# Performance work log

Measured on AMD Instinct MI355X. Metric: run time of the kernel, lower is better.

## Reference

```python
import jax, jax.numpy as jnp
import numpy as np
import math

RC = 5.0            # radial cutoff rc_rad
ZETA = [1, 2, 3, 4] # zeta list from configs['zeta']=4

def _angular_consts(z):
    # all (lx,ly,lz) with lx+ly+lz <= z (code generates n in range(z+1) and expands
    # each n into its non-negative integer triples)
    tri = []
    for lx in range(z + 1):
        for ly in range(z + 1 - lx):
            for lz in range(z + 1 - lx - ly):
                tri.append((lx, ly, lz))
    tri = np.array(tri, np.int32)
    n = tri.sum(1)
    # fact_norm = (n!/(lx!ly!lz!)) * (z!/((z-n)! n!)) = z! / ((z-n)! lx! ly! lz!)
    c = np.array([math.factorial(z) / (math.factorial(z - int(s)) * math.factorial(int(a)) * math.factorial(int(b)) * math.factorial(int(d)))
                  for (a, b, d), s in zip(tri, n)], np.float32)
    sign = ((-1.0) ** n).astype(np.float32)  # lambda=-1 channel: (1-cos)^z expansion
    return tri, c, sign

ANG = [_angular_consts(z) for z in ZETA]
silu = jax.nn.silu


def setup_inputs() -> dict:
    key = jax.random.key(0)
    ks = jax.random.split(key, 16)
    nat, npairs, Nrad, nzeta, emb, nelem = 2048, 65536, 8, 4, 4, 4
    feat = (Nrad + Nrad * 2 * nzeta) * emb  # 288
    L = 20.0
    pos = jax.random.uniform(ks[0], (nat, 3), jnp.float32) * L
    cell = L * jnp.eye(3, dtype=jnp.float32)
    i1 = jax.random.randint(ks[1], (npairs,), 0, nat, jnp.int32)
    i2 = jax.random.randint(ks[2], (npairs,), 0, nat, jnp.int32)
    shift = jnp.zeros((npairs, 3), jnp.int32)
    ids = jax.random.randint(ks[3], (nat,), 0, nelem, jnp.int32)
    onehot = jax.nn.one_hot(ids, nelem, dtype=jnp.float32)
    def W(k, i, o):
        return jax.random.normal(k, (i, o), jnp.float32) * 0.1
    return dict(
        positions=pos, cell=cell, species_onehot=onehot,
        sw1=W(ks[4], nelem, 64), sb1=jnp.zeros((64,), jnp.float32),
        sw2=W(ks[5], 64, emb), sb2=jnp.zeros((emb,), jnp.float32),
        rw1=W(ks[6], Nrad, 64), rb1=jnp.zeros((64,), jnp.float32),
        rw2=W(ks[7], 64, (nzeta + 1) * Nrad), rb2=jnp.zeros(((nzeta + 1) * Nrad,), jnp.float32),
        aw1=W(ks[8], feat, 256), ab1=jnp.zeros((256,), jnp.float32),
        aw2=W(ks[9], 256, 128), ab2=jnp.zeros((128,), jnp.float32),
        aw3=W(ks[10], 128, 1), ab3=jnp.zeros((1,), jnp.float32),
        first_atom_idx=i1, second_atom_idx=i2, shift_vectors=shift,
    )


def reference(positions, cell, species_onehot, sw1, sb1, sw2, sb2,
              rw1, rb1, rw2, rb2, aw1, ab1, aw2, ab2, aw3, ab3,
              first_atom_idx, second_atom_idx, shift_vectors):
    nat = positions.shape[0]
    Nrad = rw1.shape[0]
    nzeta = rw2.shape[1] // Nrad - 1
    # pair displacement vectors with PBC shifts
    rij = (positions[second_atom_idx] - positions[first_atom_idx]
           + shift_vectors.astype(jnp.float32) @ cell)            # [P,3]
    r = jnp.sqrt(jnp.sum(rij * rij, axis=-1) + 1e-12)             # [P]
    u = rij / r[:, None]                                          # unit vectors
    fc = jnp.where(r < RC, 0.5 * (jnp.cos(jnp.pi * r / RC) + 1.0), 0.0)
    # Gaussian radial basis -> learned radial functions (silu MLP, linear head)
    centers = jnp.linspace(0.0, RC, Nrad)
    w = RC / Nrad
    basis = jnp.exp(-((r[:, None] - centers) ** 2) / (2.0 * w * w)) * fc[:, None]
    rad = silu(basis @ rw1 + rb1) @ rw2 + rb2
    rad = rad.reshape(-1, nzeta + 1, Nrad) * fc[:, None, None]    # [P, nzeta+1, Nrad]
    # species encoder MLP -> per-atom embedding, gathered onto neighbor side
    semb = silu(species_onehot @ sw1 + sb1) @ sw2 + sb2           # [nat, emb]
    sp = semb[second_atom_idx]                                    # [P, emb]
    seg = lambda v: jax.ops.segment_sum(v, first_atom_idx, num_segments=nat)
    # two-body radial descriptor [nat, Nrad, emb]
    R = seg(rad[:, 0, :, None] * sp[:, None, :])
    feats = [R.reshape(nat, -1)]
    # three-body angular descriptors via multinomial (lx,ly,lz) expansion
    for zi in range(nzeta):
        tri, c, sign = ANG[zi]
        l = jnp.asarray(tri, jnp.float32)                         # [L,3]
        g = jnp.prod(u[:, None, :] ** l[None], axis=-1)           # [P,L] u^lx u^ly u^lz
        t = rad[:, 1 + zi, :, None, None] * g[:, None, :, None] * sp[:, None, None, :]
        G = seg(t)                                                # [nat,Nrad,L,emb]
        G2 = G * G
        Ap = jnp.einsum('inle,l->ine', G2, jnp.asarray(c))        # sum_jk f f (1+cos)^z
        Am = jnp.einsum('inle,l->ine', G2, jnp.asarray(c * sign)) # sum_jk f f (1-cos)^z
        feats += [Ap.reshape(nat, -1), Am.reshape(nat, -1)]
    F = jnp.concatenate(feats, axis=-1)                           # [nat, feature_size]
    h = silu(F @ aw1 + ab1)
    h = silu(h @ aw2 + ab2)
    e = h @ aw3 + ab3                                             # per-atom energies
    return jnp.sum(e)


if __name__ == '__main__':
    out = reference(**setup_inputs())
    print(out)
```

## Files before the change

### kernel.cpp

```cpp
#include <hip/hip_runtime.h>
#include <cmath>

#define NAT  2048
#define NP   65536
#define CAP  64
#define SCAP 8192
#define SSTR 120

__constant__ int GLX[70] = {0,
  0,0,0,1,
  0,0,0,0,0,0,1,1,1,2,
  0,0,0,0,0,0,0,0,0,0,1,1,1,1,1,1,2,2,2,3,
  0,0,0,0,0,0,0,0,0,0,0,0,0,0,0,1,1,1,1,1,1,1,1,1,1,2,2,2,2,2,2,3,3,3,4};
__constant__ int GLY[70] = {0,
  0,0,1,0,
  0,0,0,1,1,2,0,0,1,0,
  0,0,0,0,1,1,1,2,2,3,0,0,0,1,1,2,0,0,1,0,
  0,0,0,0,0,1,1,1,1,2,2,2,3,3,4,0,0,0,0,1,1,1,2,2,3,0,0,0,1,1,2,0,0,1,0};
__constant__ int GLZ[70] = {0,
  0,1,0,0,
  0,1,2,0,1,0,0,1,0,0,
  0,1,2,3,0,1,2,0,1,0,0,1,2,0,1,0,0,1,0,0,
  0,1,2,3,4,0,1,2,3,0,1,2,0,1,0,0,1,2,3,0,1,2,0,1,0,0,1,2,0,1,0,0,1,0,0};
__constant__ float C_ALL[69] = {
  1,1,1,1,
  1,2,1,2,2,1,2,2,2,1,
  1,3,3,1,3,6,3,3,3,1,3,6,3,6,6,3,3,3,3,1,
  1,4,6,4,1,4,12,12,4,6,12,6,4,4,1,4,12,12,4,12,24,12,12,12,4,6,12,6,12,12,6,4,4,4,1};
__constant__ float CS_ALL[69] = {
  1,-1,-1,-1,
  1,-2,1,-2,2,1,-2,2,2,1,
  1,-3,3,-1,-3,6,-3,3,-3,-1,-3,6,-3,6,-6,-3,3,-3,-3,-1,
  1,-4,6,-4,1,-4,12,-12,4,6,-12,6,-4,4,1,-4,12,-12,4,12,-24,12,-12,12,6,-12,6,-12,12,6,-4,4,4,1};
__constant__ int LTAB[4]    = {4,10,20,35};
__constant__ int CUMTAB[4]  = {0,4,14,34};
__constant__ int BASETAB[4] = {32,160,480,1120};

__device__ __forceinline__ float silu_f(float x){ return x / (1.0f + expf(-x)); }

__global__ __launch_bounds__(256) void k_prep(
    const float* __restrict__ pos, const float* __restrict__ cell,
    const int* __restrict__ i1, const int* __restrict__ i2,
    const int* __restrict__ sv,
    int* __restrict__ cursor, int* __restrict__ order,
    int* __restrict__ nflat, int2* __restrict__ flat)
{
  const int p = blockIdx.x*256 + threadIdx.x;
  const int a = i1[p], b = i2[p];
  const float s0=(float)sv[p*3+0], s1=(float)sv[p*3+1], s2=(float)sv[p*3+2];
  const float rx = pos[b*3+0]-pos[a*3+0] + s0*cell[0]+s1*cell[3]+s2*cell[6];
  const float ry = pos[b*3+1]-pos[a*3+1] + s0*cell[1]+s1*cell[4]+s2*cell[7];
  const float rz = pos[b*3+2]-pos[a*3+2] + s0*cell[2]+s1*cell[5]+s2*cell[8];
  const float r = sqrtf(rx*rx+ry*ry+rz*rz + 1e-12f);
  if (r < 5.0f){
    int s = atomicAdd(&cursor[a], 1);
    if (s < CAP){
      order[a*CAP + s] = p;
      int fs = atomicAdd(nflat, 1);
      if (fs < SCAP) flat[fs] = make_int2(p, a*CAP + s);
    }
  }
}

__global__ __launch_bounds__(64) void k_stage(
    const float* __restrict__ pos, const float* __restrict__ cell,
    const float* __restrict__ oneh,
    const int* __restrict__ i1, const int* __restrict__ i2,
    const int* __restrict__ sv,
    const float* __restrict__ sw1, const float* __restrict__ sb1,
    const float* __restrict__ sw2, const float* __restrict__ sb2,
    const float* __restrict__ rw1, const float* __restrict__ rb1,
    const float* __restrict__ rw2, const float* __restrict__ rb2,
    const int* __restrict__ nflat, const int2* __restrict__ flat,
    float* __restrict__ staged)
{
  const int lane = threadIdx.x;
  int ntot = *nflat; if (ntot > SCAP) ntot = SCAP;

  for (int w = blockIdx.x; w < ntot; w += 2048){
    const int2 fl = flat[w];
    const int pid = fl.x, dest = fl.y;
    const int a = i1[pid], b = i2[pid];
    const float s0=(float)sv[pid*3+0], s1=(float)sv[pid*3+1], s2=(float)sv[pid*3+2];
    const float rx = pos[b*3+0]-pos[a*3+0] + s0*cell[0]+s1*cell[3]+s2*cell[6];
    const float ry = pos[b*3+1]-pos[a*3+1] + s0*cell[1]+s1*cell[4]+s2*cell[7];
    const float rz = pos[b*3+2]-pos[a*3+2] + s0*cell[2]+s1*cell[5]+s2*cell[8];
    const float r  = sqrtf(rx*rx+ry*ry+rz*rz + 1e-12f);
    const float inv= 1.0f/r;
    const float ux=rx*inv, uy=ry*inv, uz=rz*inv;
    const float fc = 0.5f*(cosf(0.6283185307179586f*r)+1.0f);

    float basis[8];
#pragma unroll
    for (int kk=0;kk<8;kk++){
      float d = r - (float)kk*(5.0f/7.0f);
      basis[kk] = expf(-d*d*1.28f)*fc;
    }
    float h = rb1[lane];
#pragma unroll
    for (int kk=0;kk<8;kk++) h += basis[kk]*rw1[kk*64+lane];
    h = silu_f(h);
    const int ln = (lane < 40) ? lane : 0;
    float racc = rb2[ln];
#pragma unroll
    for (int o=0;o<64;o++){
      float hb = __shfl(h, o);
      racc += hb * rw2[o*40 + ln];
    }
    float* dst = staged + (size_t)dest*SSTR;
    if (lane < 40) dst[lane] = racc*fc;

    {
      int ex=GLX[lane], ey=GLY[lane], ez=GLZ[lane];
      float g=1.f;
      for (int q=0;q<ex;q++) g*=ux;
      for (int q=0;q<ey;q++) g*=uy;
      for (int q=0;q<ez;q++) g*=uz;
      dst[40+lane]=g;
    }
    if (lane < 6){
      int l2 = 64+lane;
      int ex=GLX[l2], ey=GLY[l2], ez=GLZ[l2];
      float g=1.f;
      for (int q=0;q<ex;q++) g*=ux;
      for (int q=0;q<ey;q++) g*=uy;
      for (int q=0;q<ez;q++) g*=uz;
      dst[104+lane]=g;
    }
    {
      const float o1=oneh[b*4+1], o2=oneh[b*4+2], o3=oneh[b*4+3];
      const int spec = (int)(o1 + 2.0f*o2 + 3.0f*o3 + 0.5f);
      float hh = silu_f(sb1[lane] + sw1[spec*64+lane]);
      const float4 w2 = ((const float4*)sw2)[lane];
      float q0=hh*w2.x, q1=hh*w2.y, q2=hh*w2.z, q3=hh*w2.w;
#pragma unroll
      for (int off=32; off>0; off>>=1){
        q0 += __shfl_xor(q0, off); q1 += __shfl_xor(q1, off);
        q2 += __shfl_xor(q2, off); q3 += __shfl_xor(q3, off);
      }
      if (lane < 4){
        float v = (lane==0) ? q0+sb2[0] : (lane==1) ? q1+sb2[1]
                : (lane==2) ? q2+sb2[2] : q3+sb2[3];
        dst[110+lane] = v;
      }
    }
  }
}

__global__ __launch_bounds__(256) void k_feat(
    const int* __restrict__ cursor, const int* __restrict__ order,
    const float* __restrict__ staged, float* __restrict__ Fout)
{
  const int atom = blockIdx.x, tid = threadIdx.x;
  __shared__ float G[2240];
  __shared__ float sdata[8][SSTR];
  __shared__ int opid[CAP];
  __shared__ int plist[CAP];

  int cnt = cursor[atom]; if (cnt > CAP) cnt = CAP;
  if (tid < CAP) opid[tid] = (tid < cnt) ? order[atom*CAP + tid] : 0x7fffffff;
  __syncthreads();
  if (tid < cnt){
    int my = opid[tid]; int rk = 0;
    for (int j=0;j<cnt;j++) rk += (opid[j] < my);
    plist[rk] = tid;
  }

  float acc[9];
  int ridx[9], gidx[9], eidx[9];
#pragma unroll
  for (int k=0;k<9;k++){
    acc[k]=0.f;
    int a = tid + (k<<8);
    int ri=0, gi=0, ei=0;
    if (a < 32){ ri = a>>2; gi = 0; ei = a&3; }
    else if (a < 2240){
      int b = a-32; int lb, nl, l, n;
      if (b < 128)      { lb=b;      ei=lb&3; nl=lb>>2; l=nl%4;  n=nl/4;  ri=8 +n; gi=1 +l; }
      else if (b < 448) { lb=b-128;  ei=lb&3; nl=lb>>2; l=nl%10; n=nl/10; ri=16+n; gi=5 +l; }
      else if (b < 1088){ lb=b-448;  ei=lb&3; nl=lb>>2; l=nl%20; n=nl/20; ri=24+n; gi=15+l; }
      else              { lb=b-1088; ei=lb&3; nl=lb>>2; l=nl%35; n=nl/35; ri=32+n; gi=35+l; }
    }
    ridx[k]=ri; gidx[k]=gi; eidx[k]=ei;
  }
  __syncthreads();

  for (int c0=0; c0<cnt; c0+=8){
    const int nc = (cnt-c0 < 8) ? (cnt-c0) : 8;
    for (int idx=tid; idx<nc*SSTR; idx+=256){
      int jj = idx/SSTR, i = idx - jj*SSTR;
      sdata[jj][i] = staged[(size_t)(atom*CAP + plist[c0+jj])*SSTR + i];
    }
    __syncthreads();
    for (int jj=0;jj<nc;jj++){
      const float* sd = sdata[jj];
#pragma unroll
      for (int k=0;k<9;k++)
        acc[k] += sd[ridx[k]] * sd[40+gidx[k]] * sd[110+eidx[k]];
    }
    __syncthreads();
  }

#pragma unroll
  for (int k=0;k<9;k++){
    int a = tid + (k<<8);
    if (a < 2240) G[a] = acc[k];
  }
  __syncthreads();

  float* Fo = Fout + atom*288;
  if (tid < 32) Fo[tid] = G[tid];
  if (tid < 128){
    const int zi = tid>>5, n=(tid>>2)&7, e=tid&3;
    const int L = LTAB[zi], cb = CUMTAB[zi], bs = BASETAB[zi];
    float ap=0.f, am=0.f;
    for (int l=0;l<L;l++){
      float v  = G[bs + ((n*L + l)<<2) + e];
      float v2 = v*v;
      ap += C_ALL [cb+l]*v2;
      am += CS_ALL[cb+l]*v2;
    }
    Fo[32 + (zi<<6)      + (n<<2) + e] = ap;
    Fo[32 + (zi<<6) + 32 + (n<<2) + e] = am;
  }
}

__global__ __launch_bounds__(512) void k_mlp2(
    const float* __restrict__ F,
    const float* __restrict__ aw1, const float* __restrict__ ab1,
    const float* __restrict__ aw2, const float* __restrict__ ab2,
    const float* __restrict__ aw3, const float* __restrict__ ab3,
    float* __restrict__ out)
{
  const int tid = threadIdx.x;
  const int abase = blockIdx.x*8;
  __shared__ float Fs[8][288];
  __shared__ float P1[2][8][256];
  __shared__ float Hs[8][256];
  __shared__ float P2[4][8][128];
  __shared__ float Ps[8][128];
  __shared__ float es[8];

  for (int idx=tid; idx<8*288; idx+=512){
    int a = idx/288, i = idx - a*288;
    Fs[a][i] = F[(abase+a)*288 + i];
  }
  __syncthreads();

  {
    const int o = tid & 255, half = tid >> 8;
    const int i0 = half*144;
    float p1[8];
#pragma unroll
    for (int a=0;a<8;a++) p1[a]=0.f;
    for (int i=i0;i<i0+144;i++){
      float w = aw1[i*256 + o];
#pragma unroll
      for (int a=0;a<8;a++) p1[a] += Fs[a][i]*w;
    }
#pragma unroll
    for (int a=0;a<8;a++) P1[half][a][o] = p1[a];
  }
  __syncthreads();
  {
    const int o = tid & 255, half = tid >> 8;
    if (half == 0){
#pragma unroll
      for (int a=0;a<8;a++)
        Hs[a][o] = silu_f(ab1[o] + P1[0][a][o] + P1[1][a][o]);
    }
  }
  __syncthreads();

  {
    const int o = tid & 127, q = tid >> 7;
    const int i0 = q*64;
    float p2[8];
#pragma unroll
    for (int a=0;a<8;a++) p2[a]=0.f;
    for (int i=i0;i<i0+64;i++){
      float w = aw2[i*128 + o];
#pragma unroll
      for (int a=0;a<8;a++) p2[a] += Hs[a][i]*w;
    }
#pragma unroll
    for (int a=0;a<8;a++) P2[q][a][o] = p2[a];
  }
  __syncthreads();

#pragma unroll
  for (int rep=0; rep<2; rep++){
    int idx = tid + rep*512;
    int a = idx >> 7, o = idx & 127;
    float h2 = ab2[o] + P2[0][a][o] + P2[1][a][o] + P2[2][a][o] + P2[3][a][o];
    Ps[a][o] = silu_f(h2)*aw3[o];
  }
  __syncthreads();

  {
    const int wv = tid >> 6, lane = tid & 63;
    float s = Ps[wv][lane] + Ps[wv][64+lane];
    for (int off=32; off>0; off>>=1) s += __shfl_xor(s, off);
    if (lane == 0) es[wv] = s;
  }
  __syncthreads();
  if (tid == 0){
    float bsum = es[0]+es[1]+es[2]+es[3]+es[4]+es[5]+es[6]+es[7] + 8.0f*ab3[0];
    atomicAdd(out, bsum);
  }
}

extern "C" void kernel_launch(void* const* d_in, const int* in_sizes, int n_in,
                              void* d_out, int out_size, void* d_ws, size_t ws_size,
                              hipStream_t stream) {
  const float* pos  = (const float*)d_in[0];
  const float* cell = (const float*)d_in[1];
  const float* oneh = (const float*)d_in[2];
  const float* sw1  = (const float*)d_in[3];
  const float* sb1  = (const float*)d_in[4];
  const float* sw2  = (const float*)d_in[5];
  const float* sb2  = (const float*)d_in[6];
  const float* rw1  = (const float*)d_in[7];
  const float* rb1  = (const float*)d_in[8];
  const float* rw2  = (const float*)d_in[9];
  const float* rb2  = (const float*)d_in[10];
  const float* aw1  = (const float*)d_in[11];
  const float* ab1  = (const float*)d_in[12];
  const float* aw2  = (const float*)d_in[13];
  const float* ab2  = (const float*)d_in[14];
  const float* aw3  = (const float*)d_in[15];
  const float* ab3  = (const float*)d_in[16];
  const int*   i1   = (const int*)d_in[17];
  const int*   i2   = (const int*)d_in[18];
  const int*   sv   = (const int*)d_in[19];

  char* ws = (char*)d_ws;
  int*   cursor = (int*)  (ws + 0);
  int*   nflat  = (int*)  (ws + 8192);
  int*   order  = (int*)  (ws + 8448);
  int2*  flat   = (int2*) (ws + 532736);
  float* staged = (float*)(ws + 598528);
  float* F      = (float*)(ws + 4530688);

  hipMemsetAsync(cursor, 0, 8196, stream);
  hipMemsetAsync(d_out, 0, sizeof(float), stream);
  k_prep <<<NP/256, 256, 0, stream>>>(pos, cell, i1, i2, sv,
                                      cursor, order, nflat, flat);
  k_stage<<<2048,    64, 0, stream>>>(pos, cell, oneh, i1, i2, sv,
                                      sw1, sb1, sw2, sb2,
                                      rw1, rb1, rw2, rb2,
                                      nflat, flat, staged);
  k_feat <<<NAT,    256, 0, stream>>>(cursor, order, staged, F);
  k_mlp2 <<<NAT/8,  512, 0, stream>>>(F, aw1, ab1, aw2, ab2, aw3, ab3, (float*)d_out);
}
```

Before: 73.47 us.

## Fuse all stages into one cooperative persistent kernel with grid syncs

Replaces the two memsets and four kernel launches with a single cooperative kernel of 256 blocks of 512 threads. Grid-wide syncs separate the pair binning, per-pair staging, per-atom feature accumulation and MLP phases, and a final block does a deterministic reduction in place of the atomic add. Staged rows are now indexed by flat slot through a new slot-to-flat map. The aim is to remove launch and memset overhead, at the cost of grid-sync latency and lower parallelism in the feature phase, where each block now handles 8 atoms sequentially. It also edits one entry of the sign-coefficient table, which inserts a value and shifts the rest of that row.

```diff
diff --git a/kernel.cpp b/kernel.cpp
--- a/kernel.cpp
+++ b/kernel.cpp
@@ -1,5 +1,8 @@
 #include <hip/hip_runtime.h>
+#include <hip/hip_cooperative_groups.h>
 #include <cmath>
+
+namespace cg = cooperative_groups;
 
 #define NAT  2048
 #define NP   65536
@@ -31,147 +34,141 @@
   1,-1,-1,-1,
   1,-2,1,-2,2,1,-2,2,2,1,
   1,-3,3,-1,-3,6,-3,3,-3,-1,-3,6,-3,6,-6,-3,3,-3,-3,-1,
-  1,-4,6,-4,1,-4,12,-12,4,6,-12,6,-4,4,1,-4,12,-12,4,12,-24,12,-12,12,6,-12,6,-12,12,6,-4,4,4,1};
+  1,-4,6,-4,1,-4,12,-12,4,6,-12,6,-4,4,1,-4,12,-12,4,12,-24,12,-12,12,4,6,-12,6,-12,12,6,-4,4,4,1};
 __constant__ int LTAB[4]    = {4,10,20,35};
 __constant__ int CUMTAB[4]  = {0,4,14,34};
 __constant__ int BASETAB[4] = {32,160,480,1120};
 
 __device__ __forceinline__ float silu_f(float x){ return x / (1.0f + expf(-x)); }
 
-__global__ __launch_bounds__(256) void k_prep(
-    const float* __restrict__ pos, const float* __restrict__ cell,
-    const int* __restrict__ i1, const int* __restrict__ i2,
+__global__ __launch_bounds__(512) void k_all(
+    const float* __restrict__ pos,  const float* __restrict__ cell,
+    const float* __restrict__ oneh,
+    const float* __restrict__ sw1,  const float* __restrict__ sb1,
+    const float* __restrict__ sw2,  const float* __restrict__ sb2,
+    const float* __restrict__ rw1,  const float* __restrict__ rb1,
+    const float* __restrict__ rw2,  const float* __restrict__ rb2,
+    const float* __restrict__ aw1,  const float* __restrict__ ab1,
+    const float* __restrict__ aw2,  const float* __restrict__ ab2,
+    const float* __restrict__ aw3,  const float* __restrict__ ab3,
+    const int* __restrict__ i1,     const int* __restrict__ i2,
     const int* __restrict__ sv,
-    int* __restrict__ cursor, int* __restrict__ order,
-    int* __restrict__ nflat, int2* __restrict__ flat)
+    int* cursor, int* nflat, int* order, int* slot2flat, int* flat,
+    float* staged, float* partials, float* out)
 {
-  const int p = blockIdx.x*256 + threadIdx.x;
-  const int a = i1[p], b = i2[p];
-  const float s0=(float)sv[p*3+0], s1=(float)sv[p*3+1], s2=(float)sv[p*3+2];
-  const float rx = pos[b*3+0]-pos[a*3+0] + s0*cell[0]+s1*cell[3]+s2*cell[6];
-  const float ry = pos[b*3+1]-pos[a*3+1] + s0*cell[1]+s1*cell[4]+s2*cell[7];
-  const float rz = pos[b*3+2]-pos[a*3+2] + s0*cell[2]+s1*cell[5]+s2*cell[8];
-  const float r = sqrtf(rx*rx+ry*ry+rz*rz + 1e-12f);
-  if (r < 5.0f){
-    int s = atomicAdd(&cursor[a], 1);
-    if (s < CAP){
-      order[a*CAP + s] = p;
-      int fs = atomicAdd(nflat, 1);
-      if (fs < SCAP) flat[fs] = make_int2(p, a*CAP + s);
-    }
-  }
-}
-
-__global__ __launch_bounds__(64) void k_stage(
-    const float* __restrict__ pos, const float* __restrict__ cell,
-    const float* __restrict__ oneh,
-    const int* __restrict__ i1, const int* __restrict__ i2,
-    const int* __restrict__ sv,
-    const float* __restrict__ sw1, const float* __restrict__ sb1,
-    const float* __restrict__ sw2, const float* __restrict__ sb2,
-    const float* __restrict__ rw1, const float* __restrict__ rb1,
-    const float* __restrict__ rw2, const float* __restrict__ rb2,
-    const int* __restrict__ nflat, const int2* __restrict__ flat,
-    float* __restrict__ staged)
-{
-  const int lane = threadIdx.x;
-  int ntot = *nflat; if (ntot > SCAP) ntot = SCAP;
-
-  for (int w = blockIdx.x; w < ntot; w += 2048){
-    const int2 fl = flat[w];
-    const int pid = fl.x, dest = fl.y;
-    const int a = i1[pid], b = i2[pid];
-    const float s0=(float)sv[pid*3+0], s1=(float)sv[pid*3+1], s2=(float)sv[pid*3+2];
+  cg::grid_group grid = cg::this_grid();
+  const int tid = threadIdx.x, blk = blockIdx.x;
+  const int gid = blk*512 + tid;
+  __shared__ __align__(16) char smem[58368];
+
+  if (gid < NAT) cursor[gid] = 0;
+  if (gid == 0)  *nflat = 0;
+  grid.sync();
+
+  if (gid < NP){
+    const int p = gid;
+    const int a = i1[p], b = i2[p];
+    const float s0=(float)sv[p*3+0], s1=(float)sv[p*3+1], s2=(float)sv[p*3+2];
     const float rx = pos[b*3+0]-pos[a*3+0] + s0*cell[0]+s1*cell[3]+s2*cell[6];
     const float ry = pos[b*3+1]-pos[a*3+1] + s0*cell[1]+s1*cell[4]+s2*cell[7];
     const float rz = pos[b*3+2]-pos[a*3+2] + s0*cell[2]+s1*cell[5]+s2*cell[8];
-    const float r  = sqrtf(rx*rx+ry*ry+rz*rz + 1e-12f);
-    const float inv= 1.0f/r;
-    const float ux=rx*inv, uy=ry*inv, uz=rz*inv;
-    const float fc = 0.5f*(cosf(0.6283185307179586f*r)+1.0f);
-
-    float basis[8];
-#pragma unroll
-    for (int kk=0;kk<8;kk++){
-      float d = r - (float)kk*(5.0f/7.0f);
-      basis[kk] = expf(-d*d*1.28f)*fc;
-    }
-    float h = rb1[lane];
-#pragma unroll
-    for (int kk=0;kk<8;kk++) h += basis[kk]*rw1[kk*64+lane];
-    h = silu_f(h);
-    const int ln = (lane < 40) ? lane : 0;
-    float racc = rb2[ln];
-#pragma unroll
-    for (int o=0;o<64;o++){
-      float hb = __shfl(h, o);
-      racc += hb * rw2[o*40 + ln];
-    }
-    float* dst = staged + (size_t)dest*SSTR;
-    if (lane < 40) dst[lane] = racc*fc;
-
-    {
-      int ex=GLX[lane], ey=GLY[lane], ez=GLZ[lane];
-      float g=1.f;
-      for (int q=0;q<ex;q++) g*=ux;
-      for (int q=0;q<ey;q++) g*=uy;
-      for (int q=0;q<ez;q++) g*=uz;
-      dst[40+lane]=g;
-    }
-    if (lane < 6){
-      int l2 = 64+lane;
-      int ex=GLX[l2], ey=GLY[l2], ez=GLZ[l2];
-      float g=1.f;
-      for (int q=0;q<ex;q++) g*=ux;
-      for (int q=0;q<ey;q++) g*=uy;
-      for (int q=0;q<ez;q++) g*=uz;
-      dst[104+lane]=g;
-    }
-    {
-      const float o1=oneh[b*4+1], o2=oneh[b*4+2], o3=oneh[b*4+3];
-      const int spec = (int)(o1 + 2.0f*o2 + 3.0f*o3 + 0.5f);
-      float hh = silu_f(sb1[lane] + sw1[spec*64+lane]);
-      const float4 w2 = ((const float4*)sw2)[lane];
-      float q0=hh*w2.x, q1=hh*w2.y, q2=hh*w2.z, q3=hh*w2.w;
-#pragma unroll
-      for (int off=32; off>0; off>>=1){
-        q0 += __shfl_xor(q0, off); q1 += __shfl_xor(q1, off);
-        q2 += __shfl_xor(q2, off); q3 += __shfl_xor(q3, off);
-      }
-      if (lane < 4){
-        float v = (lane==0) ? q0+sb2[0] : (lane==1) ? q1+sb2[1]
-                : (lane==2) ? q2+sb2[2] : q3+sb2[3];
-        dst[110+lane] = v;
-      }
-    }
-  }
-}
-
-__global__ __launch_bounds__(256) void k_feat(
-    const int* __restrict__ cursor, const int* __restrict__ order,
-    const float* __restrict__ staged, float* __restrict__ Fout)
-{
-  const int atom = blockIdx.x, tid = threadIdx.x;
-  __shared__ float G[2240];
-  __shared__ float sdata[8][SSTR];
-  __shared__ int opid[CAP];
-  __shared__ int plist[CAP];
-
-  int cnt = cursor[atom]; if (cnt > CAP) cnt = CAP;
-  if (tid < CAP) opid[tid] = (tid < cnt) ? order[atom*CAP + tid] : 0x7fffffff;
-  __syncthreads();
-  if (tid < cnt){
-    int my = opid[tid]; int rk = 0;
-    for (int j=0;j<cnt;j++) rk += (opid[j] < my);
-    plist[rk] = tid;
-  }
-
-  float acc[9];
-  int ridx[9], gidx[9], eidx[9];
-#pragma unroll
-  for (int k=0;k<9;k++){
-    acc[k]=0.f;
-    int a = tid + (k<<8);
+    const float r = sqrtf(rx*rx+ry*ry+rz*rz + 1e-12f);
+    if (r < 5.0f){
+      int s = atomicAdd(&cursor[a], 1);
+      if (s < CAP){
+        int fs = atomicAdd(nflat, 1);
+        order[a*CAP + s] = p;
+        if (fs < SCAP){ slot2flat[a*CAP + s] = fs; flat[fs] = p; }
+        else          { slot2flat[a*CAP + s] = -1; }
+      }
+    }
+  }
+  grid.sync();
+
+  {
+    int ntot = *nflat; if (ntot > SCAP) ntot = SCAP;
+    const int lane = tid & 63;
+    const int w0 = blk*8 + (tid >> 6);
+    for (int w = w0; w < ntot; w += 2048){
+      const int pid = flat[w];
+      const int a = i1[pid], b = i2[pid];
+      const float s0=(float)sv[pid*3+0], s1=(float)sv[pid*3+1], s2=(float)sv[pid*3+2];
+      const float rx = pos[b*3+0]-pos[a*3+0] + s0*cell[0]+s1*cell[3]+s2*cell[6];
+      const float ry = pos[b*3+1]-pos[a*3+1] + s0*cell[1]+s1*cell[4]+s2*cell[7];
+      const float rz = pos[b*3+2]-pos[a*3+2] + s0*cell[2]+s1*cell[5]+s2*cell[8];
+      const float r  = sqrtf(rx*rx+ry*ry+rz*rz + 1e-12f);
+      const float inv= 1.0f/r;
+      const float ux=rx*inv, uy=ry*inv, uz=rz*inv;
+      const float fc = 0.5f*(cosf(0.6283185307179586f*r)+1.0f);
+
+      float basis[8];
+#pragma unroll
+      for (int kk=0;kk<8;kk++){
+        float d = r - (float)kk*(5.0f/7.0f);
+        basis[kk] = expf(-d*d*1.28f)*fc;
+      }
+      float h = rb1[lane];
+#pragma unroll
+      for (int kk=0;kk<8;kk++) h += basis[kk]*rw1[kk*64+lane];
+      h = silu_f(h);
+      const int ln = (lane < 40) ? lane : 0;
+      float racc = rb2[ln];
+#pragma unroll
+      for (int o=0;o<64;o++){
+        float hb = __shfl(h, o);
+        racc += hb * rw2[o*40 + ln];
+      }
+      float* dst = staged + (size_t)w*SSTR;
+      if (lane < 40) dst[lane] = racc*fc;
+      {
+        int ex=GLX[lane], ey=GLY[lane], ez=GLZ[lane];
+        float g=1.f;
+        for (int q=0;q<ex;q++) g*=ux;
+        for (int q=0;q<ey;q++) g*=uy;
+        for (int q=0;q<ez;q++) g*=uz;
+        dst[40+lane]=g;
+      }
+      if (lane < 6){
+        int l2 = 64+lane;
+        int ex=GLX[l2], ey=GLY[l2], ez=GLZ[l2];
+        float g=1.f;
+        for (int q=0;q<ex;q++) g*=ux;
+        for (int q=0;q<ey;q++) g*=uy;
+        for (int q=0;q<ez;q++) g*=uz;
+        dst[104+lane]=g;
+      }
+      {
+        const float o1=oneh[b*4+1], o2=oneh[b*4+2], o3=oneh[b*4+3];
+        const int spec = (int)(o1 + 2.0f*o2 + 3.0f*o3 + 0.5f);
+        float hh = silu_f(sb1[lane] + sw1[spec*64+lane]);
+        const float4 w2 = ((const float4*)sw2)[lane];
+        float q0=hh*w2.x, q1=hh*w2.y, q2=hh*w2.z, q3=hh*w2.w;
+#pragma unroll
+        for (int off=32; off>0; off>>=1){
+          q0 += __shfl_xor(q0, off); q1 += __shfl_xor(q1, off);
+          q2 += __shfl_xor(q2, off); q3 += __shfl_xor(q3, off);
+        }
+        if (lane < 4){
+          float v = (lane==0) ? q0+sb2[0] : (lane==1) ? q1+sb2[1]
+                  : (lane==2) ? q2+sb2[2] : q3+sb2[3];
+          dst[110+lane] = v;
+        }
+      }
+    }
+  }
+  grid.sync();
+
+  float* G    = (float*)(smem);
+  float* sbuf = (float*)(smem+8960);
+  int*   opid = (int*)  (smem+12800);
+  int*   pslot= (int*)  (smem+13056);
+  int*   sflb = (int*)  (smem+13312);
+  float* Fs   = (float*)(smem+16384);
+
+  int ridx[5], gidx[5], eidx[5];
+#pragma unroll
+  for (int k=0;k<5;k++){
+    int a = tid + (k<<9);
     int ri=0, gi=0, ei=0;
     if (a < 32){ ri = a>>2; gi = 0; ei = a&3; }
     else if (a < 2240){
@@ -183,69 +180,69 @@
     }
     ridx[k]=ri; gidx[k]=gi; eidx[k]=ei;
   }
-  __syncthreads();
-
-  for (int c0=0; c0<cnt; c0+=8){
-    const int nc = (cnt-c0 < 8) ? (cnt-c0) : 8;
-    for (int idx=tid; idx<nc*SSTR; idx+=256){
-      int jj = idx/SSTR, i = idx - jj*SSTR;
-      sdata[jj][i] = staged[(size_t)(atom*CAP + plist[c0+jj])*SSTR + i];
-    }
-    __syncthreads();
-    for (int jj=0;jj<nc;jj++){
-      const float* sd = sdata[jj];
-#pragma unroll
-      for (int k=0;k<9;k++)
-        acc[k] += sd[ridx[k]] * sd[40+gidx[k]] * sd[110+eidx[k]];
-    }
-    __syncthreads();
-  }
-
-#pragma unroll
-  for (int k=0;k<9;k++){
-    int a = tid + (k<<8);
-    if (a < 2240) G[a] = acc[k];
-  }
-  __syncthreads();
-
-  float* Fo = Fout + atom*288;
-  if (tid < 32) Fo[tid] = G[tid];
-  if (tid < 128){
-    const int zi = tid>>5, n=(tid>>2)&7, e=tid&3;
-    const int L = LTAB[zi], cb = CUMTAB[zi], bs = BASETAB[zi];
-    float ap=0.f, am=0.f;
-    for (int l=0;l<L;l++){
-      float v  = G[bs + ((n*L + l)<<2) + e];
-      float v2 = v*v;
-      ap += C_ALL [cb+l]*v2;
-      am += CS_ALL[cb+l]*v2;
-    }
-    Fo[32 + (zi<<6)      + (n<<2) + e] = ap;
-    Fo[32 + (zi<<6) + 32 + (n<<2) + e] = am;
-  }
-}
-
-__global__ __launch_bounds__(512) void k_mlp2(
-    const float* __restrict__ F,
-    const float* __restrict__ aw1, const float* __restrict__ ab1,
-    const float* __restrict__ aw2, const float* __restrict__ ab2,
-    const float* __restrict__ aw3, const float* __restrict__ ab3,
-    float* __restrict__ out)
-{
-  const int tid = threadIdx.x;
-  const int abase = blockIdx.x*8;
-  __shared__ float Fs[8][288];
-  __shared__ float P1[2][8][256];
-  __shared__ float Hs[8][256];
-  __shared__ float P2[4][8][128];
-  __shared__ float Ps[8][128];
-  __shared__ float es[8];
-
-  for (int idx=tid; idx<8*288; idx+=512){
-    int a = idx/288, i = idx - a*288;
-    Fs[a][i] = F[(abase+a)*288 + i];
-  }
-  __syncthreads();
+
+  for (int aa=0; aa<8; aa++){
+    const int atom = blk*8 + aa;
+    int cnt = cursor[atom]; if (cnt > CAP) cnt = CAP;
+    if (tid < CAP) opid[tid] = (tid < cnt) ? order[atom*CAP + tid] : 0x7fffffff;
+    __syncthreads();
+    if (tid < cnt){
+      int my = opid[tid]; int rk = 0;
+      for (int j=0;j<cnt;j++) rk += (opid[j] < my);
+      pslot[rk] = tid;
+    }
+    float acc[5] = {0.f,0.f,0.f,0.f,0.f};
+    __syncthreads();
+
+    for (int c0=0; c0<cnt; c0+=8){
+      const int nc = (cnt-c0 < 8) ? (cnt-c0) : 8;
+      if (tid < nc) sflb[tid] = slot2flat[atom*CAP + pslot[c0+tid]];
+      __syncthreads();
+      for (int idx=tid; idx<nc*SSTR; idx+=512){
+        int jj = idx/SSTR, i = idx - jj*SSTR;
+        int fsl = sflb[jj];
+        sbuf[idx] = (fsl >= 0) ? staged[(size_t)fsl*SSTR + i] : 0.f;
+      }
+      __syncthreads();
+      for (int jj=0;jj<nc;jj++){
+        const float* sd = sbuf + jj*SSTR;
+#pragma unroll
+        for (int k=0;k<5;k++)
+          acc[k] += sd[ridx[k]] * sd[40+gidx[k]] * sd[110+eidx[k]];
+      }
+      __syncthreads();
+    }
+
+#pragma unroll
+    for (int k=0;k<5;k++){
+      int a = tid + (k<<9);
+      if (a < 2240) G[a] = acc[k];
+    }
+    __syncthreads();
+
+    float* Fo = Fs + aa*288;
+    if (tid < 32) Fo[tid] = G[tid];
+    if (tid < 128){
+      const int zi = tid>>5, n=(tid>>2)&7, e=tid&3;
+      const int L = LTAB[zi], cb = CUMTAB[zi], bs = BASETAB[zi];
+      float ap=0.f, am=0.f;
+      for (int l=0;l<L;l++){
+        float v  = G[bs + ((n*L + l)<<2) + e];
+        float v2 = v*v;
+        ap += C_ALL [cb+l]*v2;
+        am += CS_ALL[cb+l]*v2;
+      }
+      Fo[32 + (zi<<6)      + (n<<2) + e] = ap;
+      Fo[32 + (zi<<6) + 32 + (n<<2) + e] = am;
+    }
+    __syncthreads();
+  }
+
+  float* P1 = (float*)(smem+25600);
+  float* Hs = (float*)(smem);
+  float* P2 = (float*)(smem+41984);
+  float* Ps = (float*)(smem+8192);
+  float* es = (float*)(smem+12288);
 
   {
     const int o = tid & 255, half = tid >> 8;
@@ -256,10 +253,10 @@
     for (int i=i0;i<i0+144;i++){
       float w = aw1[i*256 + o];
 #pragma unroll
-      for (int a=0;a<8;a++) p1[a] += Fs[a][i]*w;
-    }
-#pragma unroll
-    for (int a=0;a<8;a++) P1[half][a][o] = p1[a];
+      for (int a=0;a<8;a++) p1[a] += Fs[a*288+i]*w;
+    }
+#pragma unroll
+    for (int a=0;a<8;a++) P1[half*2048 + a*256 + o] = p1[a];
   }
   __syncthreads();
   {
@@ -267,11 +264,10 @@
     if (half == 0){
 #pragma unroll
       for (int a=0;a<8;a++)
-        Hs[a][o] = silu_f(ab1[o] + P1[0][a][o] + P1[1][a][o]);
-    }
-  }
-  __syncthreads();
-
+        Hs[a*256+o] = silu_f(ab1[o] + P1[a*256+o] + P1[2048 + a*256+o]);
+    }
+  }
+  __syncthreads();
   {
     const int o = tid & 127, q = tid >> 7;
     const int i0 = q*64;
@@ -281,32 +277,42 @@
     for (int i=i0;i<i0+64;i++){
       float w = aw2[i*128 + o];
 #pragma unroll
-      for (int a=0;a<8;a++) p2[a] += Hs[a][i]*w;
-    }
-#pragma unroll
-    for (int a=0;a<8;a++) P2[q][a][o] = p2[a];
-  }
-  __syncthreads();
-
+      for (int a=0;a<8;a++) p2[a] += Hs[a*256+i]*w;
+    }
+#pragma unroll
+    for (int a=0;a<8;a++) P2[q*1024 + a*128 + o] = p2[a];
+  }
+  __syncthreads();
 #pragma unroll
   for (int rep=0; rep<2; rep++){
     int idx = tid + rep*512;
     int a = idx >> 7, o = idx & 127;
-    float h2 = ab2[o] + P2[0][a][o] + P2[1][a][o] + P2[2][a][o] + P2[3][a][o];
-    Ps[a][o] = silu_f(h2)*aw3[o];
-  }
-  __syncthreads();
-
+    float h2 = ab2[o] + P2[a*128+o] + P2[1024+a*128+o]
+             + P2[2048+a*128+o] + P2[3072+a*128+o];
+    Ps[a*128+o] = silu_f(h2)*aw3[o];
+  }
+  __syncthreads();
   {
     const int wv = tid >> 6, lane = tid & 63;
-    float s = Ps[wv][lane] + Ps[wv][64+lane];
+    float s = Ps[wv*128+lane] + Ps[wv*128+64+lane];
     for (int off=32; off>0; off>>=1) s += __shfl_xor(s, off);
     if (lane == 0) es[wv] = s;
   }
   __syncthreads();
   if (tid == 0){
-    float bsum = es[0]+es[1]+es[2]+es[3]+es[4]+es[5]+es[6]+es[7] + 8.0f*ab3[0];
-    atomicAdd(out, bsum);
+    partials[blk] = es[0]+es[1]+es[2]+es[3]+es[4]+es[5]+es[6]+es[7] + 8.0f*ab3[0];
+  }
+  grid.sync();
+
+  if (blk == 0){
+    float* red = (float*)smem;
+    red[tid] = (tid < 256) ? partials[tid] : 0.f;
+    __syncthreads();
+    for (int off=256; off>0; off>>=1){
+      if (tid < off) red[tid] += red[tid+off];
+      __syncthreads();
+    }
+    if (tid == 0) out[0] = red[0];
   }
 }
 
@@ -335,21 +341,24 @@
   const int*   sv   = (const int*)d_in[19];
 
   char* ws = (char*)d_ws;
-  int*   cursor = (int*)  (ws + 0);
-  int*   nflat  = (int*)  (ws + 8192);
-  int*   order  = (int*)  (ws + 8448);
-  int2*  flat   = (int2*) (ws + 532736);
-  float* staged = (float*)(ws + 598528);
-  float* F      = (float*)(ws + 4530688);
-
-  hipMemsetAsync(cursor, 0, 8196, stream);
-  hipMemsetAsync(d_out, 0, sizeof(float), stream);
-  k_prep <<<NP/256, 256, 0, stream>>>(pos, cell, i1, i2, sv,
-                                      cursor, order, nflat, flat);
-  k_stage<<<2048,    64, 0, stream>>>(pos, cell, oneh, i1, i2, sv,
-                                      sw1, sb1, sw2, sb2,
-                                      rw1, rb1, rw2, rb2,
-                                      nflat, flat, staged);
-  k_feat <<<NAT,    256, 0, stream>>>(cursor, order, staged, F);
-  k_mlp2 <<<NAT/8,  512, 0, stream>>>(F, aw1, ab1, aw2, ab2, aw3, ab3, (float*)d_out);
+  int*   cursor    = (int*)  (ws + 0);
+  int*   nflat     = (int*)  (ws + 8192);
+  int*   order     = (int*)  (ws + 8448);
+  int*   slot2flat = (int*)  (ws + 532736);
+  int*   flat      = (int*)  (ws + 1057024);
+  float* staged    = (float*)(ws + 1089792);
+  float* partials  = (float*)(ws + 5021952);
+  float* outf      = (float*)d_out;
+
+  void* args[] = {
+    (void*)&pos, (void*)&cell, (void*)&oneh,
+    (void*)&sw1, (void*)&sb1, (void*)&sw2, (void*)&sb2,
+    (void*)&rw1, (void*)&rb1, (void*)&rw2, (void*)&rb2,
+    (void*)&aw1, (void*)&ab1, (void*)&aw2, (void*)&ab2,
+    (void*)&aw3, (void*)&ab3,
+    (void*)&i1, (void*)&i2, (void*)&sv,
+    (void*)&cursor, (void*)&nflat, (void*)&order, (void*)&slot2flat,
+    (void*)&flat, (void*)&staged, (void*)&partials, (void*)&outf
+  };
+  hipLaunchCooperativeKernel((void*)k_all, dim3(256), dim3(512), args, 0, stream);
 }
```

Result: slower. 182.9 us (+148.9%).

## Fuse pair filtering and staging into one wave-compacted kernel

Applied to the files above, without the earlier changes.

Merges the pair-filter and staging kernels. Each wavefront ballots its surviving pairs, reserves flat slots with a single atomic, and then processes the survivors by broadcasting their geometry through shuffles. The per-species embedding MLP is computed once per block into shared memory instead of once per pair. The two memsets become one, and the final float atomicAdd is replaced by a last-block reduction over per-block partials. A CS_ALL constant is also edited. In exchange, the staging work now runs on only 256 blocks, which may serialize the per-survivor MLP loop within each wave.

```diff
diff --git a/kernel.cpp b/kernel.cpp
--- a/kernel.cpp
+++ b/kernel.cpp
@@ -31,38 +31,14 @@
   1,-1,-1,-1,
   1,-2,1,-2,2,1,-2,2,2,1,
   1,-3,3,-1,-3,6,-3,3,-3,-1,-3,6,-3,6,-6,-3,3,-3,-3,-1,
-  1,-4,6,-4,1,-4,12,-12,4,6,-12,6,-4,4,1,-4,12,-12,4,12,-24,12,-12,12,6,-12,6,-12,12,6,-4,4,4,1};
+  1,-4,6,-4,1,-4,12,-12,4,6,-12,6,-4,4,1,-4,12,-12,4,12,-24,12,-12,12,4,6,-12,6,-12,12,6,-4,4,4,1};
 __constant__ int LTAB[4]    = {4,10,20,35};
 __constant__ int CUMTAB[4]  = {0,4,14,34};
 __constant__ int BASETAB[4] = {32,160,480,1120};
 
 __device__ __forceinline__ float silu_f(float x){ return x / (1.0f + expf(-x)); }
 
-__global__ __launch_bounds__(256) void k_prep(
-    const float* __restrict__ pos, const float* __restrict__ cell,
-    const int* __restrict__ i1, const int* __restrict__ i2,
-    const int* __restrict__ sv,
-    int* __restrict__ cursor, int* __restrict__ order,
-    int* __restrict__ nflat, int2* __restrict__ flat)
-{
-  const int p = blockIdx.x*256 + threadIdx.x;
-  const int a = i1[p], b = i2[p];
-  const float s0=(float)sv[p*3+0], s1=(float)sv[p*3+1], s2=(float)sv[p*3+2];
-  const float rx = pos[b*3+0]-pos[a*3+0] + s0*cell[0]+s1*cell[3]+s2*cell[6];
-  const float ry = pos[b*3+1]-pos[a*3+1] + s0*cell[1]+s1*cell[4]+s2*cell[7];
-  const float rz = pos[b*3+2]-pos[a*3+2] + s0*cell[2]+s1*cell[5]+s2*cell[8];
-  const float r = sqrtf(rx*rx+ry*ry+rz*rz + 1e-12f);
-  if (r < 5.0f){
-    int s = atomicAdd(&cursor[a], 1);
-    if (s < CAP){
-      order[a*CAP + s] = p;
-      int fs = atomicAdd(nflat, 1);
-      if (fs < SCAP) flat[fs] = make_int2(p, a*CAP + s);
-    }
-  }
-}
-
-__global__ __launch_bounds__(64) void k_stage(
+__global__ __launch_bounds__(256) void k_pairstage(
     const float* __restrict__ pos, const float* __restrict__ cell,
     const float* __restrict__ oneh,
     const int* __restrict__ i1, const int* __restrict__ i2,
@@ -71,30 +47,73 @@
     const float* __restrict__ sw2, const float* __restrict__ sb2,
     const float* __restrict__ rw1, const float* __restrict__ rb1,
     const float* __restrict__ rw2, const float* __restrict__ rb2,
-    const int* __restrict__ nflat, const int2* __restrict__ flat,
+    int* __restrict__ cursor, int* __restrict__ nflat,
+    int* __restrict__ ord_pid, int* __restrict__ ord_flat,
     float* __restrict__ staged)
 {
-  const int lane = threadIdx.x;
-  int ntot = *nflat; if (ntot > SCAP) ntot = SCAP;
-
-  for (int w = blockIdx.x; w < ntot; w += 2048){
-    const int2 fl = flat[w];
-    const int pid = fl.x, dest = fl.y;
-    const int a = i1[pid], b = i2[pid];
-    const float s0=(float)sv[pid*3+0], s1=(float)sv[pid*3+1], s2=(float)sv[pid*3+2];
-    const float rx = pos[b*3+0]-pos[a*3+0] + s0*cell[0]+s1*cell[3]+s2*cell[6];
-    const float ry = pos[b*3+1]-pos[a*3+1] + s0*cell[1]+s1*cell[4]+s2*cell[7];
-    const float rz = pos[b*3+2]-pos[a*3+2] + s0*cell[2]+s1*cell[5]+s2*cell[8];
-    const float r  = sqrtf(rx*rx+ry*ry+rz*rz + 1e-12f);
-    const float inv= 1.0f/r;
-    const float ux=rx*inv, uy=ry*inv, uz=rz*inv;
-    const float fc = 0.5f*(cosf(0.6283185307179586f*r)+1.0f);
+  __shared__ float sembs[4][4];
+  const int tid = threadIdx.x, lane = tid & 63, wid = tid >> 6;
+
+  {
+    float h = silu_f(sb1[lane] + sw1[wid*64 + lane]);
+    const float4 w2 = ((const float4*)sw2)[lane];
+    float q0=h*w2.x, q1=h*w2.y, q2=h*w2.z, q3=h*w2.w;
+#pragma unroll
+    for (int off=32; off>0; off>>=1){
+      q0 += __shfl_xor(q0, off); q1 += __shfl_xor(q1, off);
+      q2 += __shfl_xor(q2, off); q3 += __shfl_xor(q3, off);
+    }
+    if (lane < 4){
+      float v = (lane==0) ? q0+sb2[0] : (lane==1) ? q1+sb2[1]
+              : (lane==2) ? q2+sb2[2] : q3+sb2[3];
+      sembs[wid][lane] = v;
+    }
+  }
+  __syncthreads();
+
+  const int p = (blockIdx.x*4 + wid)*64 + lane;
+  const int a = i1[p], b = i2[p];
+  const float s0=(float)sv[p*3+0], s1=(float)sv[p*3+1], s2=(float)sv[p*3+2];
+  const float rx = pos[b*3+0]-pos[a*3+0] + s0*cell[0]+s1*cell[3]+s2*cell[6];
+  const float ry = pos[b*3+1]-pos[a*3+1] + s0*cell[1]+s1*cell[4]+s2*cell[7];
+  const float rz = pos[b*3+2]-pos[a*3+2] + s0*cell[2]+s1*cell[5]+s2*cell[8];
+  const float r  = sqrtf(rx*rx+ry*ry+rz*rz + 1e-12f);
+  const bool ok  = (r < 5.0f);
+  const float inv= 1.0f/r;
+  const float ux=rx*inv, uy=ry*inv, uz=rz*inv;
+  const float fcl= 0.5f*(cosf(0.6283185307179586f*r)+1.0f);
+
+  const unsigned long long mask = __ballot(ok);
+  const int nsurv = __popcll(mask);
+  if (nsurv == 0) return;
+
+  int base = 0;
+  if (lane == 0) base = atomicAdd(nflat, nsurv);
+  base = __shfl(base, 0);
+  const int rank = __popcll(mask & ((1ull<<lane)-1ull));
+  const int fs = base + rank;
+  if (ok){
+    int s = atomicAdd(&cursor[a], 1);
+    if (s < CAP){
+      ord_pid [a*CAP + s] = p;
+      ord_flat[a*CAP + s] = fs;
+    }
+  }
+
+  unsigned long long m = mask;
+  while (m){
+    const int src = __ffsll((long long)m) - 1; m &= m-1;
+    const float sux=__shfl(ux,src), suy=__shfl(uy,src), suz=__shfl(uz,src);
+    const float sr =__shfl(r ,src), sfc=__shfl(fcl,src);
+    const int   sb_=__shfl(b ,src), sfs=__shfl(fs ,src);
+    if (sfs >= SCAP) continue;
+    float* dst = staged + (size_t)sfs*SSTR;
 
     float basis[8];
 #pragma unroll
     for (int kk=0;kk<8;kk++){
-      float d = r - (float)kk*(5.0f/7.0f);
-      basis[kk] = expf(-d*d*1.28f)*fc;
+      float d = sr - (float)kk*(5.0f/7.0f);
+      basis[kk] = expf(-d*d*1.28f)*sfc;
     }
     float h = rb1[lane];
 #pragma unroll
@@ -107,63 +126,49 @@
       float hb = __shfl(h, o);
       racc += hb * rw2[o*40 + ln];
     }
-    float* dst = staged + (size_t)dest*SSTR;
-    if (lane < 40) dst[lane] = racc*fc;
-
+    if (lane < 40) dst[lane] = racc*sfc;
     {
       int ex=GLX[lane], ey=GLY[lane], ez=GLZ[lane];
       float g=1.f;
-      for (int q=0;q<ex;q++) g*=ux;
-      for (int q=0;q<ey;q++) g*=uy;
-      for (int q=0;q<ez;q++) g*=uz;
+      for (int q=0;q<ex;q++) g*=sux;
+      for (int q=0;q<ey;q++) g*=suy;
+      for (int q=0;q<ez;q++) g*=suz;
       dst[40+lane]=g;
     }
     if (lane < 6){
       int l2 = 64+lane;
       int ex=GLX[l2], ey=GLY[l2], ez=GLZ[l2];
       float g=1.f;
-      for (int q=0;q<ex;q++) g*=ux;
-      for (int q=0;q<ey;q++) g*=uy;
-      for (int q=0;q<ez;q++) g*=uz;
+      for (int q=0;q<ex;q++) g*=sux;
+      for (int q=0;q<ey;q++) g*=suy;
+      for (int q=0;q<ez;q++) g*=suz;
       dst[104+lane]=g;
     }
-    {
-      const float o1=oneh[b*4+1], o2=oneh[b*4+2], o3=oneh[b*4+3];
-      const int spec = (int)(o1 + 2.0f*o2 + 3.0f*o3 + 0.5f);
-      float hh = silu_f(sb1[lane] + sw1[spec*64+lane]);
-      const float4 w2 = ((const float4*)sw2)[lane];
-      float q0=hh*w2.x, q1=hh*w2.y, q2=hh*w2.z, q3=hh*w2.w;
-#pragma unroll
-      for (int off=32; off>0; off>>=1){
-        q0 += __shfl_xor(q0, off); q1 += __shfl_xor(q1, off);
-        q2 += __shfl_xor(q2, off); q3 += __shfl_xor(q3, off);
-      }
-      if (lane < 4){
-        float v = (lane==0) ? q0+sb2[0] : (lane==1) ? q1+sb2[1]
-                : (lane==2) ? q2+sb2[2] : q3+sb2[3];
-        dst[110+lane] = v;
-      }
-    }
+    const float o1=oneh[sb_*4+1], o2=oneh[sb_*4+2], o3=oneh[sb_*4+3];
+    const int spec = (int)(o1 + 2.0f*o2 + 3.0f*o3 + 0.5f);
+    if (lane < 4) dst[110+lane] = sembs[spec][lane];
   }
 }
 
 __global__ __launch_bounds__(256) void k_feat(
-    const int* __restrict__ cursor, const int* __restrict__ order,
+    const int* __restrict__ cursor,
+    const int* __restrict__ ord_pid, const int* __restrict__ ord_flat,
     const float* __restrict__ staged, float* __restrict__ Fout)
 {
   const int atom = blockIdx.x, tid = threadIdx.x;
   __shared__ float G[2240];
   __shared__ float sdata[8][SSTR];
   __shared__ int opid[CAP];
-  __shared__ int plist[CAP];
+  __shared__ int pslot[CAP];
+  __shared__ int sflb[8];
 
   int cnt = cursor[atom]; if (cnt > CAP) cnt = CAP;
-  if (tid < CAP) opid[tid] = (tid < cnt) ? order[atom*CAP + tid] : 0x7fffffff;
+  if (tid < CAP) opid[tid] = (tid < cnt) ? ord_pid[atom*CAP + tid] : 0x7fffffff;
   __syncthreads();
   if (tid < cnt){
     int my = opid[tid]; int rk = 0;
     for (int j=0;j<cnt;j++) rk += (opid[j] < my);
-    plist[rk] = tid;
+    pslot[rk] = tid;
   }
 
   float acc[9];
@@ -187,9 +192,12 @@
 
   for (int c0=0; c0<cnt; c0+=8){
     const int nc = (cnt-c0 < 8) ? (cnt-c0) : 8;
+    if (tid < nc) sflb[tid] = ord_flat[atom*CAP + pslot[c0+tid]];
+    __syncthreads();
     for (int idx=tid; idx<nc*SSTR; idx+=256){
       int jj = idx/SSTR, i = idx - jj*SSTR;
-      sdata[jj][i] = staged[(size_t)(atom*CAP + plist[c0+jj])*SSTR + i];
+      int fsl = sflb[jj];
+      sdata[jj][i] = (fsl < SCAP) ? staged[(size_t)fsl*SSTR + i] : 0.f;
     }
     __syncthreads();
     for (int jj=0;jj<nc;jj++){
@@ -230,6 +238,7 @@
     const float* __restrict__ aw1, const float* __restrict__ ab1,
     const float* __restrict__ aw2, const float* __restrict__ ab2,
     const float* __restrict__ aw3, const float* __restrict__ ab3,
+    float* __restrict__ partials, int* __restrict__ done,
     float* __restrict__ out)
 {
   const int tid = threadIdx.x;
@@ -240,6 +249,7 @@
   __shared__ float P2[4][8][128];
   __shared__ float Ps[8][128];
   __shared__ float es[8];
+  __shared__ int winner;
 
   for (int idx=tid; idx<8*288; idx+=512){
     int a = idx/288, i = idx - a*288;
@@ -306,7 +316,22 @@
   __syncthreads();
   if (tid == 0){
     float bsum = es[0]+es[1]+es[2]+es[3]+es[4]+es[5]+es[6]+es[7] + 8.0f*ab3[0];
-    atomicAdd(out, bsum);
+    __hip_atomic_store(&partials[blockIdx.x], bsum,
+                       __ATOMIC_RELEASE, __HIP_MEMORY_SCOPE_AGENT);
+    int old = __hip_atomic_fetch_add(done, 1, __ATOMIC_ACQ_REL,
+                                     __HIP_MEMORY_SCOPE_AGENT);
+    winner = (old == (NAT/8) - 1) ? 1 : 0;
+  }
+  __syncthreads();
+
+  if (winner && tid < 64){
+    float s = 0.f;
+#pragma unroll
+    for (int q=0;q<4;q++)
+      s += __hip_atomic_load(&partials[tid*4+q],
+                             __ATOMIC_ACQUIRE, __HIP_MEMORY_SCOPE_AGENT);
+    for (int off=32; off>0; off>>=1) s += __shfl_xor(s, off);
+    if (tid == 0) out[0] = s;
   }
 }
 
@@ -335,21 +360,21 @@
   const int*   sv   = (const int*)d_in[19];
 
   char* ws = (char*)d_ws;
-  int*   cursor = (int*)  (ws + 0);
-  int*   nflat  = (int*)  (ws + 8192);
-  int*   order  = (int*)  (ws + 8448);
-  int2*  flat   = (int2*) (ws + 532736);
-  float* staged = (float*)(ws + 598528);
-  float* F      = (float*)(ws + 4530688);
-
-  hipMemsetAsync(cursor, 0, 8196, stream);
-  hipMemsetAsync(d_out, 0, sizeof(float), stream);
-  k_prep <<<NP/256, 256, 0, stream>>>(pos, cell, i1, i2, sv,
-                                      cursor, order, nflat, flat);
-  k_stage<<<2048,    64, 0, stream>>>(pos, cell, oneh, i1, i2, sv,
-                                      sw1, sb1, sw2, sb2,
-                                      rw1, rb1, rw2, rb2,
-                                      nflat, flat, staged);
-  k_feat <<<NAT,    256, 0, stream>>>(cursor, order, staged, F);
-  k_mlp2 <<<NAT/8,  512, 0, stream>>>(F, aw1, ab1, aw2, ab2, aw3, ab3, (float*)d_out);
+  int*   cursor   = (int*)  (ws + 0);
+  int*   nflat    = (int*)  (ws + 8192);
+  int*   done     = (int*)  (ws + 8196);
+  int*   ord_pid  = (int*)  (ws + 8448);
+  int*   ord_flat = (int*)  (ws + 532736);
+  float* staged   = (float*)(ws + 1057024);
+  float* F        = (float*)(ws + 4989184);
+  float* partials = (float*)(ws + 7348480);
+
+  hipMemsetAsync(ws, 0, 8448, stream);
+  k_pairstage<<<256,  256, 0, stream>>>(pos, cell, oneh, i1, i2, sv,
+                                        sw1, sb1, sw2, sb2,
+                                        rw1, rb1, rw2, rb2,
+                                        cursor, nflat, ord_pid, ord_flat, staged);
+  k_feat     <<<NAT,  256, 0, stream>>>(cursor, ord_pid, ord_flat, staged, F);
+  k_mlp2     <<<NAT/8,512, 0, stream>>>(F, aw1, ab1, aw2, ab2, aw3, ab3,
+                                        partials, done, (float*)d_out);
 }
```

Result: slower. 109.1 us (+48.5%).
